# Kernel tuning notes

Measured on AMD Instinct MI355X. Metric: run time of the kernel, lower is better.

The kernel has to match this reference:

```python
import jax, jax.numpy as jnp
import numpy as np

B, S, D, H, W = 2, 2048, 1024, 16, 128
HD = D // H


def setup_inputs() -> dict:
    key = jax.random.key(0)
    ks = jax.random.split(key, 9)
    s = 1.0 / np.sqrt(D)
    return {
        "x": jax.random.normal(ks[0], (B, S, D), jnp.float32),
        "Wq": jax.random.normal(ks[1], (D, D), jnp.float32) * s,
        "bq": jax.random.normal(ks[2], (D,), jnp.float32) * 0.01,
        "Wk": jax.random.normal(ks[3], (D, D), jnp.float32) * s,
        "bk": jax.random.normal(ks[4], (D,), jnp.float32) * 0.01,
        "Wv": jax.random.normal(ks[5], (D, D), jnp.float32) * s,
        "bv": jax.random.normal(ks[6], (D,), jnp.float32) * 0.01,
        "Wo": jax.random.normal(ks[7], (D, D), jnp.float32) * s,
        "bo": jax.random.normal(ks[8], (D,), jnp.float32) * 0.01,
    }


def reference(x, Wq, bq, Wk, bk, Wv, bv, Wo, bo):
    b, s, d = x.shape
    # projections (torch Linear: x @ W.T + b)
    q = (jnp.einsum('bsd,ed->bse', x, Wq) + bq).reshape(b, s, H, HD).transpose(0, 2, 1, 3)
    k = (jnp.einsum('bsd,ed->bse', x, Wk) + bk).reshape(b, s, H, HD).transpose(0, 2, 1, 3)
    v = (jnp.einsum('bsd,ed->bse', x, Wv) + bv).reshape(b, s, H, HD).transpose(0, 2, 1, 3)
    scores = jnp.einsum('bhqd,bhkd->bhqk', q, k) / jnp.sqrt(jnp.asarray(HD, x.dtype))
    # local band mask: mask[i, j] = 1 iff i - W//2 <= j <= i + W//2
    idx = jnp.arange(s)
    band = jnp.abs(idx[:, None] - idx[None, :]) <= (W // 2)  # [S, S]
    scores = jnp.where(band[None, None], scores, -jnp.inf)
    attn = jax.nn.softmax(scores, axis=-1)  # dropout is identity in eval
    ctx = jnp.einsum('bhqk,bhkd->bqhd', attn, v).reshape(b, s, d)
    out = jnp.einsum('bsd,ed->bse', ctx, Wo) + bo
    return out, attn
```

## Files before the change

kernel.cpp:

```cpp
#include <hip/hip_runtime.h>
#include <math.h>
#include <stdint.h>

typedef _Float16 f16;
typedef f16   f16x8 __attribute__((ext_vector_type(8)));
typedef f16   f16x4 __attribute__((ext_vector_type(4)));
typedef float f32x4 __attribute__((ext_vector_type(4)));

constexpr int Bc = 2, Sc = 2048, Dc = 1024, Hc = 16, HDc = 64;
constexpr size_t PROJ = (size_t)Bc * Sc * Dc;
constexpr size_t WN   = (size_t)Dc * Dc;

__device__ __forceinline__ void gload_lds16(const void* g, void* l) {
    unsigned int off = (unsigned int)(uintptr_t)l;
    auto lp = (__attribute__((address_space(3))) unsigned int*)(uintptr_t)off;
    auto gp = (const __attribute__((address_space(1))) unsigned int*)(uintptr_t)g;
    __builtin_amdgcn_global_load_lds(gp, lp, 16, 0, 0);
}

__global__ __launch_bounds__(256)
void pack_x(const float* __restrict__ src, f16* __restrict__ dst) {
    const int i = blockIdx.x * 256 + threadIdx.x;
    float4 f = ((const float4*)src)[i];
    f16x4 h = {(f16)f.x, (f16)f.y, (f16)f.z, (f16)f.w};
    ((f16x4*)dst)[i] = h;
}

__global__ __launch_bounds__(256)
void pack_w(const float* __restrict__ w0, const float* __restrict__ w1,
            const float* __restrict__ w2, const float* __restrict__ w3,
            f16* __restrict__ dst) {
    const int ten = blockIdx.y;
    const float* src = (ten == 0) ? w0 : (ten == 1) ? w1 : (ten == 2) ? w2 : w3;
    f16* d = dst + (size_t)ten * WN;
    const int i = blockIdx.x * 256 + threadIdx.x;
    float4 f = ((const float4*)src)[i];
    f16x4 h = {(f16)f.x, (f16)f.y, (f16)f.z, (f16)f.w};
    ((f16x4*)d)[i] = h;
}

template <typename OutT>
__global__ __launch_bounds__(256, 2)
void gemm_f16(const f16* __restrict__ A, const f16* __restrict__ W,
              const float* __restrict__ b0, const float* __restrict__ b1,
              const float* __restrict__ b2,
              OutT* __restrict__ o0, OutT* __restrict__ o1, OutT* __restrict__ o2) {
    constexpr int K = 1024, N = 1024;
    __shared__ f16 sA[128 * 32];
    __shared__ f16 sB[64 * 32];

    const int t = threadIdx.x;
    const int w = t >> 6, l = t & 63, l15 = l & 15, quad = l >> 4;
    const int row0 = blockIdx.y * 128, col0 = blockIdx.x * 64;
    const int wr = w >> 1, wc = w & 1;

    f32x4 acc[4][2];
    #pragma unroll
    for (int i = 0; i < 4; ++i)
        #pragma unroll
        for (int j = 0; j < 2; ++j) acc[i][j] = (f32x4){0.f, 0.f, 0.f, 0.f};

    const int arow = t >> 2;
    const int koff = (t & 3) * 8;
    const f16* ga = A + (size_t)(row0 + arow) * K + koff;
    const f16* gb = W + (size_t)(col0 + arow) * K + koff;
    f16* lA1 = sA + w * 512;
    f16* lA2 = sA + 2048 + w * 512;
    f16* lB1 = sB + w * 512;

    for (int k0 = 0; k0 < K; k0 += 32) {
        gload_lds16(ga + k0, lA1);
        gload_lds16(ga + 64 * K + k0, lA2);
        gload_lds16(gb + k0, lB1);
        __syncthreads();

        f16x8 ah[4], bh[2];
        #pragma unroll
        for (int mi = 0; mi < 4; ++mi)
            ah[mi] = *(const f16x8*)&sA[(wr * 64 + mi * 16 + l15) * 32 + quad * 8];
        #pragma unroll
        for (int ni = 0; ni < 2; ++ni)
            bh[ni] = *(const f16x8*)&sB[(wc * 32 + ni * 16 + l15) * 32 + quad * 8];
        #pragma unroll
        for (int mi = 0; mi < 4; ++mi)
            #pragma unroll
            for (int ni = 0; ni < 2; ++ni)
                acc[mi][ni] = __builtin_amdgcn_mfma_f32_16x16x32_f16(ah[mi], bh[ni], acc[mi][ni], 0, 0, 0);
        __syncthreads();
    }

    const int ten = col0 >> 10;
    const float* bias = (ten == 0) ? b0 : (ten == 1) ? b1 : b2;
    OutT* out = (ten == 0) ? o0 : (ten == 1) ? o1 : o2;
    const int nc0 = col0 & (N - 1);

    #pragma unroll
    for (int mi = 0; mi < 4; ++mi)
        #pragma unroll
        for (int ni = 0; ni < 2; ++ni) {
            const int rbase = row0 + wr * 64 + mi * 16 + quad * 4;
            const int col = nc0 + wc * 32 + ni * 16 + l15;
            const float bv = bias[col];
            #pragma unroll
            for (int r = 0; r < 4; ++r)
                out[(size_t)(rbase + r) * N + col] = (OutT)(acc[mi][ni][r] + bv);
        }
}

__global__ __launch_bounds__(256, 2)
void attn_fused(const f16* __restrict__ qb, const f16* __restrict__ kb,
                const f16* __restrict__ vb, float* __restrict__ attn,
                f16* __restrict__ ctx) {
    __shared__ f16 sQ[64 * 72];
    __shared__ f16 sK[192 * 72];
    __shared__ f16 sV[192 * 72];
    f16* sP = sK;

    const int t = threadIdx.x, w = t >> 6, l = t & 63, l15 = l & 15, quad = l >> 4;
    const int bx = blockIdx.x;
    const int tile = bx & 31, h = (bx >> 5) & 15, b = bx >> 9;
    const int q0 = tile * 64;
    const int jbase = q0 - 64;

    const f16* qg = qb + ((size_t)(b * Sc + q0)) * Dc + h * HDc;
    #pragma unroll
    for (int it = 0; it < 2; ++it) {
        const int idx = it * 256 + t;
        const int r = idx >> 3, c = (idx & 7) * 8;
        *(uint4*)&sQ[r * 72 + c] = *(const uint4*)&qg[(size_t)r * Dc + c];
    }
    #pragma unroll
    for (int it = 0; it < 6; ++it) {
        const int idx = it * 256 + t;
        const int r = idx >> 3, c = (idx & 7) * 8;
        int j = jbase + r;
        j = (j < 0) ? 0 : (j > Sc - 1 ? Sc - 1 : j);
        const size_t goff = ((size_t)(b * Sc + j)) * Dc + h * HDc + c;
        *(uint4*)&sK[r * 72 + c] = *(const uint4*)&kb[goff];
        *(uint4*)&sV[r * 72 + c] = *(const uint4*)&vb[goff];
    }
    __syncthreads();

    float* abase = attn + ((size_t)(b * Hc + h) * Sc) * Sc;
    {
        uint4* z = (uint4*)(abase + (size_t)q0 * Sc);
        const uint4 zero = {0u, 0u, 0u, 0u};
        for (int it = 0; it < 128; ++it)
            z[it * 256 + t] = zero;
    }

    f32x4 s[12];
    #pragma unroll
    for (int nt = 0; nt < 12; ++nt) s[nt] = (f32x4){0.f, 0.f, 0.f, 0.f};
    #pragma unroll
    for (int kk = 0; kk < 64; kk += 32) {
        const f16x8 aq = *(const f16x8*)&sQ[(w * 16 + l15) * 72 + kk + quad * 8];
        #pragma unroll
        for (int nt = 0; nt < 12; ++nt) {
            const f16x8 bk_ = *(const f16x8*)&sK[(nt * 16 + l15) * 72 + kk + quad * 8];
            s[nt] = __builtin_amdgcn_mfma_f32_16x16x32_f16(aq, bk_, s[nt], 0, 0, 0);
        }
    }

    float invr[4];
    #pragma unroll
    for (int r = 0; r < 4; ++r) {
        const int row = w * 16 + quad * 4 + r;
        const int lo = (row > 64 - q0) ? row : (64 - q0);
        const int hi2 = (row + 128 < 2111 - q0) ? (row + 128) : (2111 - q0);
        float m = -1e30f;
        #pragma unroll
        for (int nt = 0; nt < 12; ++nt) {
            const int jrel = nt * 16 + l15;
            const float v = s[nt][r] * 0.125f;
            if (jrel >= lo && jrel <= hi2) m = fmaxf(m, v);
        }
        #pragma unroll
        for (int k = 1; k < 16; k <<= 1) m = fmaxf(m, __shfl_xor(m, k, 64));
        float sum = 0.f;
        #pragma unroll
        for (int nt = 0; nt < 12; ++nt) {
            const int jrel = nt * 16 + l15;
            const float v = s[nt][r] * 0.125f;
            const float e = (jrel >= lo && jrel <= hi2) ? __expf(v - m) : 0.f;
            s[nt][r] = e;
            sum += e;
        }
        #pragma unroll
        for (int k = 1; k < 16; k <<= 1) sum += __shfl_xor(sum, k, 64);
        invr[r] = 1.f / sum;
    }
    __syncthreads();

    #pragma unroll
    for (int r = 0; r < 4; ++r) {
        const int row = w * 16 + quad * 4 + r;
        const int i = q0 + row;
        const int lo = (row > 64 - q0) ? row : (64 - q0);
        const int hi2 = (row + 128 < 2111 - q0) ? (row + 128) : (2111 - q0);
        #pragma unroll
        for (int nt = 0; nt < 12; ++nt) {
            const int jrel = nt * 16 + l15;
            const float p = s[nt][r] * invr[r];
            sP[row * 200 + jrel] = (f16)p;
            if (jrel >= lo && jrel <= hi2)
                abase[(size_t)i * Sc + (jbase + jrel)] = p;
        }
    }
    __syncthreads();

    f32x4 o[4];
    #pragma unroll
    for (int dt = 0; dt < 4; ++dt) o[dt] = (f32x4){0.f, 0.f, 0.f, 0.f};
    #pragma unroll
    for (int ks = 0; ks < 6; ++ks) {
        const f16x8 ap = *(const f16x8*)&sP[(w * 16 + l15) * 200 + ks * 32 + quad * 8];
        #pragma unroll
        for (int dt = 0; dt < 4; ++dt) {
            f16x8 bv;
            #pragma unroll
            for (int jj = 0; jj < 8; ++jj)
                bv[jj] = sV[(ks * 32 + quad * 8 + jj) * 72 + dt * 16 + l15];
            o[dt] = __builtin_amdgcn_mfma_f32_16x16x32_f16(ap, bv, o[dt], 0, 0, 0);
        }
    }
    f16* cg = ctx + ((size_t)(b * Sc + q0)) * Dc + h * HDc;
    #pragma unroll
    for (int dt = 0; dt < 4; ++dt)
        #pragma unroll
        for (int r = 0; r < 4; ++r) {
            const int row = w * 16 + quad * 4 + r;
            cg[(size_t)row * Dc + dt * 16 + l15] = (f16)o[dt][r];
        }
}

extern "C" void kernel_launch(void* const* d_in, const int* in_sizes, int n_in,
                              void* d_out, int out_size, void* d_ws, size_t ws_size,
                              hipStream_t stream) {
    const float* x  = (const float*)d_in[0];
    const float* Wq = (const float*)d_in[1];
    const float* bq = (const float*)d_in[2];
    const float* Wk = (const float*)d_in[3];
    const float* bk = (const float*)d_in[4];
    const float* Wv = (const float*)d_in[5];
    const float* bv = (const float*)d_in[6];
    const float* Wo = (const float*)d_in[7];
    const float* bo = (const float*)d_in[8];

    float* out  = (float*)d_out;
    float* attn = out + PROJ;

    char* ws = (char*)d_ws;
    f16* Wcat  = (f16*)ws;
    f16* x_f16 = (f16*)(ws + (size_t)8  * 1024 * 1024);
    f16* q_f16 = (f16*)(ws + (size_t)16 * 1024 * 1024);
    f16* k_f16 = (f16*)(ws + (size_t)24 * 1024 * 1024);
    f16* v_f16 = (f16*)(ws + (size_t)32 * 1024 * 1024);
    f16* c_f16 = (f16*)(ws + (size_t)40 * 1024 * 1024);

    pack_x<<<dim3(PROJ / 1024), dim3(256), 0, stream>>>(x, x_f16);
    pack_w<<<dim3(WN / 1024, 4), dim3(256), 0, stream>>>(Wq, Wk, Wv, Wo, Wcat);

    gemm_f16<f16><<<dim3(48, 32), dim3(256), 0, stream>>>(
        x_f16, Wcat, bq, bk, bv, q_f16, k_f16, v_f16);

    attn_fused<<<dim3(Bc * Hc * (Sc / 64)), dim3(256), 0, stream>>>(
        q_f16, k_f16, v_f16, attn, c_f16);

    gemm_f16<float><<<dim3(16, 32), dim3(256), 0, stream>>>(
        c_f16, Wcat + 3 * WN, bo, bo, bo, out, out, out);
}
```

Baseline: 666.1 us.

## Overlap attention zero-fill with QKV GEMM, enlarge GEMM tiles, merge pack kernels

The zeroing of the dense attention-probability output moves out of the attention kernel into extra blocks of the QKV projection GEMM launch. The bandwidth-bound fill can then run alongside the compute-bound matmul, and the attention kernel only writes the band values. The GEMM tile grows from 128x64 to 128x128 on a 1D grid, which gives more reuse per LDS load but raises register use and leaves fewer blocks. The two fp32-to-fp16 pack kernels are merged into one launch.

```diff
diff --git a/kernel.cpp b/kernel.cpp
--- a/kernel.cpp
+++ b/kernel.cpp
@@ -19,46 +19,62 @@
 }
 
 __global__ __launch_bounds__(256)
-void pack_x(const float* __restrict__ src, f16* __restrict__ dst) {
-    const int i = blockIdx.x * 256 + threadIdx.x;
+void pack_all(const float* __restrict__ x,
+              const float* __restrict__ w0, const float* __restrict__ w1,
+              const float* __restrict__ w2, const float* __restrict__ w3,
+              f16* __restrict__ xd, f16* __restrict__ wd) {
+    const int bid = blockIdx.x;
+    const float* src;
+    f16* dst;
+    int off4;
+    if (bid < 4096) {
+        src = x; dst = xd; off4 = bid;
+    } else {
+        const int wi = (bid - 4096) >> 10;
+        const int r  = (bid - 4096) & 1023;
+        src = (wi == 0) ? w0 : (wi == 1) ? w1 : (wi == 2) ? w2 : w3;
+        dst = wd + (size_t)wi * WN;
+        off4 = r;
+    }
+    const int i = off4 * 256 + threadIdx.x;
     float4 f = ((const float4*)src)[i];
     f16x4 h = {(f16)f.x, (f16)f.y, (f16)f.z, (f16)f.w};
     ((f16x4*)dst)[i] = h;
 }
 
-__global__ __launch_bounds__(256)
-void pack_w(const float* __restrict__ w0, const float* __restrict__ w1,
-            const float* __restrict__ w2, const float* __restrict__ w3,
-            f16* __restrict__ dst) {
-    const int ten = blockIdx.y;
-    const float* src = (ten == 0) ? w0 : (ten == 1) ? w1 : (ten == 2) ? w2 : w3;
-    f16* d = dst + (size_t)ten * WN;
-    const int i = blockIdx.x * 256 + threadIdx.x;
-    float4 f = ((const float4*)src)[i];
-    f16x4 h = {(f16)f.x, (f16)f.y, (f16)f.z, (f16)f.w};
-    ((f16x4*)d)[i] = h;
-}
-
 template <typename OutT>
 __global__ __launch_bounds__(256, 2)
-void gemm_f16(const f16* __restrict__ A, const f16* __restrict__ W,
-              const float* __restrict__ b0, const float* __restrict__ b1,
-              const float* __restrict__ b2,
-              OutT* __restrict__ o0, OutT* __restrict__ o1, OutT* __restrict__ o2) {
+void gemm_mega(const f16* __restrict__ A, const f16* __restrict__ W,
+               const float* __restrict__ b0, const float* __restrict__ b1,
+               const float* __restrict__ b2,
+               OutT* __restrict__ o0, OutT* __restrict__ o1, OutT* __restrict__ o2,
+               float* __restrict__ fill, int n_gemm, int n_ct) {
     constexpr int K = 1024, N = 1024;
+    const int bid = blockIdx.x;
+    const int t = threadIdx.x;
+
+    if (bid >= n_gemm) {
+        uint4* z = (uint4*)fill + (size_t)(bid - n_gemm) * 16384;
+        const uint4 zero = {0u, 0u, 0u, 0u};
+        #pragma unroll 8
+        for (int it = 0; it < 64; ++it)
+            z[it * 256 + t] = zero;
+        return;
+    }
+
     __shared__ f16 sA[128 * 32];
-    __shared__ f16 sB[64 * 32];
-
-    const int t = threadIdx.x;
+    __shared__ f16 sB[128 * 32];
+
     const int w = t >> 6, l = t & 63, l15 = l & 15, quad = l >> 4;
-    const int row0 = blockIdx.y * 128, col0 = blockIdx.x * 64;
+    const int col_t = bid % n_ct, row_t = bid / n_ct;
+    const int row0 = row_t * 128, col0 = col_t * 128;
     const int wr = w >> 1, wc = w & 1;
 
-    f32x4 acc[4][2];
+    f32x4 acc[4][4];
     #pragma unroll
     for (int i = 0; i < 4; ++i)
         #pragma unroll
-        for (int j = 0; j < 2; ++j) acc[i][j] = (f32x4){0.f, 0.f, 0.f, 0.f};
+        for (int j = 0; j < 4; ++j) acc[i][j] = (f32x4){0.f, 0.f, 0.f, 0.f};
 
     const int arow = t >> 2;
     const int koff = (t & 3) * 8;
@@ -67,25 +83,27 @@
     f16* lA1 = sA + w * 512;
     f16* lA2 = sA + 2048 + w * 512;
     f16* lB1 = sB + w * 512;
+    f16* lB2 = sB + 2048 + w * 512;
 
     for (int k0 = 0; k0 < K; k0 += 32) {
         gload_lds16(ga + k0, lA1);
-        gload_lds16(ga + 64 * K + k0, lA2);
+        gload_lds16(ga + (size_t)64 * K + k0, lA2);
         gload_lds16(gb + k0, lB1);
+        gload_lds16(gb + (size_t)64 * K + k0, lB2);
         __syncthreads();
 
-        f16x8 ah[4], bh[2];
+        f16x8 af[4], bf[4];
         #pragma unroll
         for (int mi = 0; mi < 4; ++mi)
-            ah[mi] = *(const f16x8*)&sA[(wr * 64 + mi * 16 + l15) * 32 + quad * 8];
-        #pragma unroll
-        for (int ni = 0; ni < 2; ++ni)
-            bh[ni] = *(const f16x8*)&sB[(wc * 32 + ni * 16 + l15) * 32 + quad * 8];
+            af[mi] = *(const f16x8*)&sA[(wr * 64 + mi * 16 + l15) * 32 + quad * 8];
+        #pragma unroll
+        for (int ni = 0; ni < 4; ++ni)
+            bf[ni] = *(const f16x8*)&sB[(wc * 64 + ni * 16 + l15) * 32 + quad * 8];
         #pragma unroll
         for (int mi = 0; mi < 4; ++mi)
             #pragma unroll
-            for (int ni = 0; ni < 2; ++ni)
-                acc[mi][ni] = __builtin_amdgcn_mfma_f32_16x16x32_f16(ah[mi], bh[ni], acc[mi][ni], 0, 0, 0);
+            for (int ni = 0; ni < 4; ++ni)
+                acc[mi][ni] = __builtin_amdgcn_mfma_f32_16x16x32_f16(af[mi], bf[ni], acc[mi][ni], 0, 0, 0);
         __syncthreads();
     }
 
@@ -97,9 +115,9 @@
     #pragma unroll
     for (int mi = 0; mi < 4; ++mi)
         #pragma unroll
-        for (int ni = 0; ni < 2; ++ni) {
+        for (int ni = 0; ni < 4; ++ni) {
             const int rbase = row0 + wr * 64 + mi * 16 + quad * 4;
-            const int col = nc0 + wc * 32 + ni * 16 + l15;
+            const int col = nc0 + wc * 64 + ni * 16 + l15;
             const float bv = bias[col];
             #pragma unroll
             for (int r = 0; r < 4; ++r)
@@ -141,14 +159,6 @@
     }
     __syncthreads();
 
-    float* abase = attn + ((size_t)(b * Hc + h) * Sc) * Sc;
-    {
-        uint4* z = (uint4*)(abase + (size_t)q0 * Sc);
-        const uint4 zero = {0u, 0u, 0u, 0u};
-        for (int it = 0; it < 128; ++it)
-            z[it * 256 + t] = zero;
-    }
-
     f32x4 s[12];
     #pragma unroll
     for (int nt = 0; nt < 12; ++nt) s[nt] = (f32x4){0.f, 0.f, 0.f, 0.f};
@@ -192,6 +202,7 @@
     }
     __syncthreads();
 
+    float* abase = attn + ((size_t)(b * Hc + h) * Sc) * Sc;
     #pragma unroll
     for (int r = 0; r < 4; ++r) {
         const int row = w * 16 + quad * 4 + r;
@@ -258,15 +269,14 @@
     f16* v_f16 = (f16*)(ws + (size_t)32 * 1024 * 1024);
     f16* c_f16 = (f16*)(ws + (size_t)40 * 1024 * 1024);
 
-    pack_x<<<dim3(PROJ / 1024), dim3(256), 0, stream>>>(x, x_f16);
-    pack_w<<<dim3(WN / 1024, 4), dim3(256), 0, stream>>>(Wq, Wk, Wv, Wo, Wcat);
-
-    gemm_f16<f16><<<dim3(48, 32), dim3(256), 0, stream>>>(
-        x_f16, Wcat, bq, bk, bv, q_f16, k_f16, v_f16);
+    pack_all<<<dim3(8192), dim3(256), 0, stream>>>(x, Wq, Wk, Wv, Wo, x_f16, Wcat);
+
+    gemm_mega<f16><<<dim3(768 + 2048), dim3(256), 0, stream>>>(
+        x_f16, Wcat, bq, bk, bv, q_f16, k_f16, v_f16, attn, 768, 24);
 
     attn_fused<<<dim3(Bc * Hc * (Sc / 64)), dim3(256), 0, stream>>>(
         q_f16, k_f16, v_f16, attn, c_f16);
 
-    gemm_f16<float><<<dim3(16, 32), dim3(256), 0, stream>>>(
-        c_f16, Wcat + 3 * WN, bo, bo, bo, out, out, out);
-}
+    gemm_mega<float><<<dim3(256), dim3(256), 0, stream>>>(
+        c_f16, Wcat + 3 * WN, bo, bo, bo, out, out, out, nullptr, 256, 8);
+}
```

Result: no change. 661.3 us (-0.7%).
